# Optimization experiments

Hardware: AMD Instinct MI355X
Metric: run time of the kernel (lower is better)

## Reference

```python
import jax, jax.numpy as jnp
import numpy as np

H = 16
D_MODEL = 1024
D_K = D_MODEL // H


def setup_inputs() -> dict:
    key = jax.random.key(0)
    ks = jax.random.split(key, 12)
    B, S = 2, 2048
    scale = 1.0 / np.sqrt(D_MODEL)
    inp = {
        "query": jax.random.normal(ks[0], (B, S, D_MODEL), jnp.float32),
        "key": jax.random.normal(ks[1], (B, S, D_MODEL), jnp.float32),
        "value": jax.random.normal(ks[2], (B, S, D_MODEL), jnp.float32),
        "mask": jnp.ones((B, 1, S), jnp.int32),
        "Wq": jax.random.normal(ks[3], (D_MODEL, D_MODEL), jnp.float32) * scale,
        "bq": jnp.zeros((D_MODEL,), jnp.float32),
        "Wk": jax.random.normal(ks[4], (D_MODEL, D_MODEL), jnp.float32) * scale,
        "bk": jnp.zeros((D_MODEL,), jnp.float32),
        "Wv": jax.random.normal(ks[5], (D_MODEL, D_MODEL), jnp.float32) * scale,
        "bv": jnp.zeros((D_MODEL,), jnp.float32),
        "Wo": jax.random.normal(ks[6], (D_MODEL, D_MODEL), jnp.float32) * scale,
        "bo": jnp.zeros((D_MODEL,), jnp.float32),
    }
    return inp


def reference(query, key, value, mask, Wq, bq, Wk, bk, Wv, bv, Wo, bo):
    B, S, _ = query.shape
    # QKV projections, split heads: [B, S, D] -> [B, H, S, d_k]
    def proj(x, W, b):
        y = x @ W.T + b
        return y.reshape(B, -1, H, D_K).transpose(0, 2, 1, 3)

    q = proj(query, Wq, bq)
    k = proj(key, Wk, bk)
    v = proj(value, Wv, bv)

    # scaled dot-product attention with full score matrix [B, H, Sq, Sk]
    scores = jnp.einsum("bhqd,bhkd->bhqk", q, k) / np.sqrt(D_K)
    m = mask[:, None, :, :]  # unsqueeze head dim: [B, 1, 1_or_S, S]
    scores = jnp.where(m == 0, jnp.float32(-1e9), scores)
    p_attn = jax.nn.softmax(scores, axis=-1)  # dropout p=0.0 (eval)
    x = jnp.einsum("bhqk,bhkd->bhqd", p_attn, v)

    # merge heads and output projection
    x = x.transpose(0, 2, 1, 3).reshape(B, -1, H * D_K)
    return x @ Wo.T + bo
```

## Files before the change

### kernel.cpp

```cpp
#include <hip/hip_runtime.h>
#include <hip/hip_bf16.h>
#include <stdint.h>

typedef unsigned short us;
typedef __bf16 bf8 __attribute__((ext_vector_type(8)));
typedef float  f4  __attribute__((ext_vector_type(4)));

typedef unsigned int __attribute__((address_space(1))) as1_uint;
typedef unsigned int __attribute__((address_space(3))) as3_uint;

__device__ __forceinline__ void async_ld16(const void* g, void* l) {
    __builtin_amdgcn_global_load_lds((as1_uint*)g, (as3_uint*)l, 16, 0, 0);
}

__device__ __forceinline__ us f2bf(float f) {
    __hip_bfloat16 h = __float2bfloat16(f);
    us u;
    __builtin_memcpy(&u, &h, 2);
    return u;
}

__device__ __forceinline__ unsigned cvt_pk_bf16(float lo, float hi) {
    unsigned r;
    asm("v_cvt_pk_bf16_f32 %0, %1, %2" : "=v"(r) : "v"(lo), "v"(hi));
    return r;
}

__device__ __forceinline__ float fexp2(float x) {
#if __has_builtin(__builtin_amdgcn_exp2f)
    return __builtin_amdgcn_exp2f(x);
#else
    return exp2f(x);
#endif
}

#define SCALE_Q 0.18033688011112042f

__global__ __launch_bounds__(256)
void convert_all(const float* __restrict__ s0, const float* __restrict__ s1,
                 const float* __restrict__ s2, const float* __restrict__ s3,
                 const float* __restrict__ s4, const float* __restrict__ s5,
                 const float* __restrict__ s6,
                 us* __restrict__ d0, us* __restrict__ d1, us* __restrict__ d2,
                 us* __restrict__ d3, us* __restrict__ d4, us* __restrict__ d5,
                 us* __restrict__ d6)
{
    size_t i4 = (((size_t)blockIdx.x * 256) + threadIdx.x) << 2;
    const float* src; us* dst; size_t off;
    if (i4 < ((size_t)3 << 22)) {
        unsigned seg = (unsigned)(i4 >> 22);
        off = i4 & (((size_t)1 << 22) - 1);
        src = seg == 0 ? s0 : (seg == 1 ? s1 : s2);
        dst = seg == 0 ? d0 : (seg == 1 ? d1 : d2);
    } else {
        size_t j = i4 - ((size_t)3 << 22);
        unsigned seg = (unsigned)(j >> 20);
        off = j & (((size_t)1 << 20) - 1);
        src = seg == 0 ? s3 : (seg == 1 ? s4 : (seg == 2 ? s5 : s6));
        dst = seg == 0 ? d3 : (seg == 1 ? d4 : (seg == 2 ? d5 : d6));
    }
    float4 f = *(const float4*)(src + off);
    ushort4 o;
    o.x = f2bf(f.x); o.y = f2bf(f.y); o.z = f2bf(f.z); o.w = f2bf(f.w);
    *(ushort4*)(dst + off) = o;
}

template<int MODE, int BN>
__device__ __forceinline__
void gemm_body(const us* __restrict__ A, const us* __restrict__ W,
               const float* __restrict__ bias, void* __restrict__ out,
               float scale, int bx, int by)
{
    __shared__ us lA[128 * 32];
    __shared__ us lB[BN * 32];

    const int tid  = threadIdx.x;
    const int wv   = tid >> 6;
    const int lane = tid & 63;
    const int l15  = lane & 15;
    const int quad = lane >> 4;
    const int kq   = quad << 3;
    const int cr   = quad << 2;
    const int srow = lane >> 2;
    const int scol = (lane & 3) << 3;
    const int m0   = by << 7;
    const int n0   = bx * BN;
    constexpr int MJ = (BN == 128) ? 4 : 2;
    const int wm = (BN == 128) ? ((wv >> 1) << 6) : (wv << 5);
    const int wn = (BN == 128) ? ((wv & 1) << 6) : 0;

    f4 acc[4][MJ];
    const f4 zero = {0.f, 0.f, 0.f, 0.f};
#pragma unroll
    for (int i = 0; i < 4; ++i)
#pragma unroll
        for (int j = 0; j < MJ; ++j) acc[i][j] = zero;

    for (int kt = 0; kt < 1024; kt += 32) {
#pragma unroll
        for (int s = 0; s < 2; ++s) {
            const int chunk = wv * 2 + s;
            const int row   = chunk * 16 + srow;
            async_ld16(A + (size_t)(m0 + row) * 1024 + kt + scol, &lA[chunk * 512]);
        }
        if (BN == 128) {
#pragma unroll
            for (int s = 0; s < 2; ++s) {
                const int chunk = wv * 2 + s;
                const int row   = chunk * 16 + srow;
                async_ld16(W + (size_t)(n0 + row) * 1024 + kt + scol, &lB[chunk * 512]);
            }
        } else {
            const int row = wv * 16 + srow;
            async_ld16(W + (size_t)(n0 + row) * 1024 + kt + scol, &lB[wv * 512]);
        }
        __syncthreads();

        bf8 wf[4], xf[MJ];
#pragma unroll
        for (int i = 0; i < 4; ++i)
            wf[i] = *(const bf8*)&lB[(wn + i * 16 + l15) * 32 + kq];
#pragma unroll
        for (int j = 0; j < MJ; ++j)
            xf[j] = *(const bf8*)&lA[(wm + j * 16 + l15) * 32 + kq];
#pragma unroll
        for (int i = 0; i < 4; ++i)
#pragma unroll
            for (int j = 0; j < MJ; ++j)
                acc[i][j] = __builtin_amdgcn_mfma_f32_16x16x32_bf16(wf[i], xf[j], acc[i][j], 0, 0, 0);
        __syncthreads();
    }

    if (MODE == 2) {
        us* o = (us*)out;
#pragma unroll
        for (int j = 0; j < MJ; ++j) {
            const int f = m0 + wm + j * 16 + l15;
            const float bf_ = bias[f];
            const int hh = f >> 6, dd = f & 63;
#pragma unroll
            for (int i = 0; i < 4; ++i) {
                const int tokb = n0 + wn + i * 16 + cr;
                const int bb = tokb >> 11, ss_phys = tokb & 2047;
                const int k6 = ss_phys & 63;
                const int kt6 = k6 >> 4, qd = (k6 >> 2) & 3;
                const int c6 = ((kt6 >> 1) << 5) | (qd << 3) | ((kt6 & 1) << 2);
                const int ss = (ss_phys & ~63) | c6;
                us hp[4];
#pragma unroll
                for (int r = 0; r < 4; ++r) hp[r] = f2bf(acc[i][j][r] + bf_);
                uint2 w;
                w.x = (unsigned)hp[0] | ((unsigned)hp[1] << 16);
                w.y = (unsigned)hp[2] | ((unsigned)hp[3] << 16);
                *(uint2*)&o[((size_t)((bb * 16 + hh) * 64 + dd) << 11) + ss] = w;
            }
        }
        return;
    }

#pragma unroll
    for (int i = 0; i < 4; ++i) {
        const int gnb = n0 + wn + i * 16 + cr;
        const f4 bj = *(const f4*)&bias[gnb];
        if (MODE == 0) {
            us* o = (us*)out;
            const int hh = gnb >> 6, dd = gnb & 63;
#pragma unroll
            for (int j = 0; j < MJ; ++j) {
                const int gm = m0 + wm + j * 16 + l15;
                const int bb = gm >> 11, ss = gm & 2047;
                us hp[4];
#pragma unroll
                for (int r = 0; r < 4; ++r)
                    hp[r] = f2bf((acc[i][j][r] + bj[r]) * scale);
                uint2 w;
                w.x = (unsigned)hp[0] | ((unsigned)hp[1] << 16);
                w.y = (unsigned)hp[2] | ((unsigned)hp[3] << 16);
                *(uint2*)&o[(((size_t)(bb * 16 + hh) * 2048 + ss) << 6) + dd] = w;
            }
        } else {
            float* o = (float*)out;
#pragma unroll
            for (int j = 0; j < MJ; ++j) {
                const int gm = m0 + wm + j * 16 + l15;
                f4 v;
#pragma unroll
                for (int r = 0; r < 4; ++r) v[r] = acc[i][j][r] + bj[r];
                *(f4*)&o[((size_t)gm << 10) + gnb] = v;
            }
        }
    }
}

__global__ __launch_bounds__(256)
void gemm_qkv(const us* __restrict__ XQ, const us* __restrict__ XK,
              const us* __restrict__ XV,
              const us* __restrict__ WQ, const us* __restrict__ WK,
              const us* __restrict__ WV,
              const float* __restrict__ bq, const float* __restrict__ bk,
              const float* __restrict__ bv,
              us* __restrict__ QP, us* __restrict__ KP, us* __restrict__ VT)
{
    const int z = blockIdx.z;
    if (z == 2) {
        gemm_body<2, 128>(WV, XV, bv, VT, 1.0f, blockIdx.y, blockIdx.x);
        return;
    }
    const us* A = z == 0 ? XQ : XK;
    const us* W = z == 0 ? WQ : WK;
    const float* b = z == 0 ? bq : bk;
    us* o = z == 0 ? QP : KP;
    const float scale = z == 0 ? SCALE_Q : 1.0f;
    gemm_body<0, 128>(A, W, b, o, scale, blockIdx.x, blockIdx.y);
}

__global__ __launch_bounds__(256)
void gemm_o(const us* __restrict__ A, const us* __restrict__ W,
            const float* __restrict__ bias, float* __restrict__ out)
{
    gemm_body<1, 64>(A, W, bias, out, 1.0f, blockIdx.x, blockIdx.y);
}

__global__ __launch_bounds__(512)
void flash_attn(const us* __restrict__ Qp, const us* __restrict__ Kp,
                const us* __restrict__ Vtp, const int* __restrict__ maskp,
                us* __restrict__ ctx)
{
    __shared__ us lK[2][64 * 64];
    __shared__ us lVt[2][64 * 64];
    __shared__ float lmask[2][64];

    const int tid  = threadIdx.x;
    const int wv   = tid >> 6;
    const int lane = tid & 63;
    const int l15  = lane & 15;
    const int quad = lane >> 4;
    const int cr   = quad << 2;
    const int l7   = l15 & 7;

    const int q0 = blockIdx.x << 8;
    const int h  = blockIdx.y;
    const int b  = blockIdx.z;

    const size_t headoff = ((size_t)(b * 16 + h)) << 17;
    const us* Qh  = Qp  + headoff;
    const us* Kh  = Kp  + headoff;
    const us* Vth = Vtp + headoff;

    const int gr    = lane >> 3;
    const int gslot = ((lane & 7) ^ gr) << 3;

    bf8 qf[2][2];
#pragma unroll
    for (int nt = 0; nt < 2; ++nt)
#pragma unroll
        for (int kb = 0; kb < 2; ++kb)
            qf[nt][kb] = *(const bf8*)(Qh + ((size_t)(q0 + wv * 32 + nt * 16 + l15) << 6)
                                          + kb * 32 + (quad << 3));

    const f4 zero = {0.f, 0.f, 0.f, 0.f};
    f4 of[4][2];
#pragma unroll
    for (int dt = 0; dt < 4; ++dt)
#pragma unroll
        for (int nt = 0; nt < 2; ++nt) of[dt][nt] = zero;
    float li[2] = {0.f, 0.f};

#define FA_ISSUE(kt0, bi)                                                      \
    {                                                                          \
        const int rbase = wv * 8;                                              \
        const int r = rbase + gr;                                              \
        async_ld16(Kh + ((size_t)((kt0) + r) << 6) + gslot,                    \
                   &lK[bi][rbase * 64]);                                       \
        async_ld16(Vth + (size_t)r * 2048 + (kt0) + gslot,                     \
                   &lVt[bi][rbase * 64]);                                      \
        if (tid < 64)                                                          \
            lmask[bi][tid] =                                                   \
                (maskp[((size_t)b << 11) + (kt0) + tid] == 0) ? 0.0f : 1.0f;   \
    }

    FA_ISSUE(0, 0);

    for (int t = 0; t < 32; ++t) {
        const int cur = t & 1;
        __syncthreads();
        if (t < 31) FA_ISSUE((t + 1) * 64, cur ^ 1);

        const us* lKc  = lK[cur];
        const us* lVtc = lVt[cur];

        float rs[2] = {0.f, 0.f};
        unsigned pkx[4][2], pky[4][2];
        __builtin_amdgcn_s_setprio(1);
#pragma unroll
        for (int kt = 0; kt < 4; ++kt) {
            const int krow = (kt * 16 + l15) << 6;
            bf8 kf0 = *(const bf8*)&lKc[krow + ((quad ^ l7) << 3)];
            bf8 kf1 = *(const bf8*)&lKc[krow + (((4 + quad) ^ l7) << 3)];
            f4 st[2];
#pragma unroll
            for (int nt = 0; nt < 2; ++nt) {
                st[nt] = __builtin_amdgcn_mfma_f32_16x16x32_bf16(kf0, qf[nt][0], zero, 0, 0, 0);
                st[nt] = __builtin_amdgcn_mfma_f32_16x16x32_bf16(kf1, qf[nt][1], st[nt], 0, 0, 0);
            }
            const f4 mr = *(const f4*)&lmask[cur][kt * 16 + cr];
#pragma unroll
            for (int nt = 0; nt < 2; ++nt) {
                float p[4];
#pragma unroll
                for (int r = 0; r < 4; ++r) {
                    p[r] = fexp2(st[nt][r]) * mr[r];
                    rs[nt] += p[r];
                }
                pkx[kt][nt] = cvt_pk_bf16(p[0], p[1]);
                pky[kt][nt] = cvt_pk_bf16(p[2], p[3]);
            }
        }
        __builtin_amdgcn_s_setprio(0);
#pragma unroll
        for (int nt = 0; nt < 2; ++nt) {
            float r2 = rs[nt];
            r2 += __shfl_xor(r2, 16, 64);
            r2 += __shfl_xor(r2, 32, 64);
            li[nt] += r2;
        }

        __builtin_amdgcn_s_setprio(1);
#pragma unroll
        for (int kb = 0; kb < 2; ++kb) {
            bf8 pfr[2];
#pragma unroll
            for (int nt = 0; nt < 2; ++nt) {
                uint4 u;
                u.x = pkx[2 * kb][nt];
                u.y = pky[2 * kb][nt];
                u.z = pkx[2 * kb + 1][nt];
                u.w = pky[2 * kb + 1][nt];
                __builtin_memcpy(&pfr[nt], &u, 16);
            }
#pragma unroll
            for (int dt = 0; dt < 4; ++dt) {
                bf8 vf = *(const bf8*)&lVtc[((dt * 16 + l15) << 6) + (((kb * 4 + quad) ^ l7) << 3)];
#pragma unroll
                for (int nt = 0; nt < 2; ++nt)
                    of[dt][nt] = __builtin_amdgcn_mfma_f32_16x16x32_bf16(vf, pfr[nt], of[dt][nt], 0, 0, 0);
            }
        }
        __builtin_amdgcn_s_setprio(0);
    }
#undef FA_ISSUE

#pragma unroll
    for (int nt = 0; nt < 2; ++nt) {
        const float linv = 1.0f / li[nt];
        const int tok = q0 + wv * 32 + nt * 16 + l15;
        const size_t rowb = (((size_t)(b * 2048 + tok)) << 10) + (h << 6);
#pragma unroll
        for (int dt = 0; dt < 4; ++dt) {
            uint2 w;
            w.x = cvt_pk_bf16(of[dt][nt][0] * linv, of[dt][nt][1] * linv);
            w.y = cvt_pk_bf16(of[dt][nt][2] * linv, of[dt][nt][3] * linv);
            *(uint2*)&ctx[rowb + dt * 16 + cr] = w;
        }
    }
}

extern "C" void kernel_launch(void* const* d_in, const int* in_sizes, int n_in,
                              void* d_out, int out_size, void* d_ws, size_t ws_size,
                              hipStream_t stream)
{
    const float* q    = (const float*)d_in[0];
    const float* k    = (const float*)d_in[1];
    const float* v    = (const float*)d_in[2];
    const int*   mask = (const int*)d_in[3];
    const float* Wq   = (const float*)d_in[4];
    const float* bq   = (const float*)d_in[5];
    const float* Wk   = (const float*)d_in[6];
    const float* bk   = (const float*)d_in[7];
    const float* Wv   = (const float*)d_in[8];
    const float* bv   = (const float*)d_in[9];
    const float* Wo   = (const float*)d_in[10];
    const float* bo   = (const float*)d_in[11];
    float* out = (float*)d_out;

    us* ws  = (us*)d_ws;
    us* XQ  = ws;
    us* XK  = ws + 4194304;
    us* XV  = ws + 8388608;
    us* WQb = ws + 12582912;
    us* WKb = ws + 13631488;
    us* WVb = ws + 14680064;
    us* WOb = ws + 15728640;
    us* QP  = ws + 16777216;
    us* KP  = ws + 20971520;
    us* VT  = ws + 25165824;
    us* CTX = XQ;

    convert_all<<<16384, 256, 0, stream>>>(q, k, v, Wq, Wk, Wv, Wo,
                                           XQ, XK, XV, WQb, WKb, WVb, WOb);
    gemm_qkv<<<dim3(8, 32, 3), 256, 0, stream>>>(XQ, XK, XV, WQb, WKb, WVb,
                                                 bq, bk, bv, QP, KP, VT);
    flash_attn<<<dim3(8, 16, 2), 512, 0, stream>>>(QP, KP, VT, mask, CTX);
    gemm_o<<<dim3(16, 32), 256, 0, stream>>>(CTX, WOb, bo, out);
}
```

Measured before the change: 233.3 us.

## Deepen flash-attention K/V pipeline to four LDS stages with vmcnt-based waits

Moves the K/Vt staging in flash_attn from double to quadruple buffering, prefetching two tiles ahead. It replaces __syncthreads with an explicit s_waitcnt vmcnt plus s_barrier, so each wave waits only for the oldest outstanding loads. The whole mask row is converted to float and preloaded into LDS once at kernel start, and the s_setprio hints are dropped. This raises LDS use per block, which may lower occupancy, and the correctness of the vmcnt counts depends on async load ordering.

```diff
diff --git a/kernel.cpp b/kernel.cpp
--- a/kernel.cpp
+++ b/kernel.cpp
@@ -226,9 +226,9 @@
                 const us* __restrict__ Vtp, const int* __restrict__ maskp,
                 us* __restrict__ ctx)
 {
-    __shared__ us lK[2][64 * 64];
-    __shared__ us lVt[2][64 * 64];
-    __shared__ float lmask[2][64];
+    __shared__ us lK[4][64 * 64];
+    __shared__ us lVt[4][64 * 64];
+    __shared__ float lmaskA[2048];
 
     const int tid  = threadIdx.x;
     const int wv   = tid >> 6;
@@ -249,6 +249,16 @@
 
     const int gr    = lane >> 3;
     const int gslot = ((lane & 7) ^ gr) << 3;
+
+    {
+        const int4 mi = *(const int4*)(maskp + ((size_t)b << 11) + (tid << 2));
+        float4 mf;
+        mf.x = mi.x == 0 ? 0.0f : 1.0f;
+        mf.y = mi.y == 0 ? 0.0f : 1.0f;
+        mf.z = mi.z == 0 ? 0.0f : 1.0f;
+        mf.w = mi.w == 0 ? 0.0f : 1.0f;
+        *(float4*)&lmaskA[tid << 2] = mf;
+    }
 
     bf8 qf[2][2];
 #pragma unroll
@@ -274,24 +284,26 @@
                    &lK[bi][rbase * 64]);                                       \
         async_ld16(Vth + (size_t)r * 2048 + (kt0) + gslot,                     \
                    &lVt[bi][rbase * 64]);                                      \
-        if (tid < 64)                                                          \
-            lmask[bi][tid] =                                                   \
-                (maskp[((size_t)b << 11) + (kt0) + tid] == 0) ? 0.0f : 1.0f;   \
-    }
+    }
+
+    __syncthreads();
 
     FA_ISSUE(0, 0);
+    FA_ISSUE(64, 1);
 
     for (int t = 0; t < 32; ++t) {
-        const int cur = t & 1;
-        __syncthreads();
-        if (t < 31) FA_ISSUE((t + 1) * 64, cur ^ 1);
-
-        const us* lKc  = lK[cur];
-        const us* lVtc = lVt[cur];
+        if (t < 31) asm volatile("s_waitcnt vmcnt(2)" ::: "memory");
+        else        asm volatile("s_waitcnt vmcnt(0)" ::: "memory");
+        __builtin_amdgcn_s_barrier();
+        __builtin_amdgcn_sched_barrier(0);
+        if (t < 30) FA_ISSUE((t + 2) * 64, (t + 2) & 3);
+
+        const us* lKc  = lK[t & 3];
+        const us* lVtc = lVt[t & 3];
+        const float* lmt = &lmaskA[t << 6];
 
         float rs[2] = {0.f, 0.f};
         unsigned pkx[4][2], pky[4][2];
-        __builtin_amdgcn_s_setprio(1);
 #pragma unroll
         for (int kt = 0; kt < 4; ++kt) {
             const int krow = (kt * 16 + l15) << 6;
@@ -303,7 +315,7 @@
                 st[nt] = __builtin_amdgcn_mfma_f32_16x16x32_bf16(kf0, qf[nt][0], zero, 0, 0, 0);
                 st[nt] = __builtin_amdgcn_mfma_f32_16x16x32_bf16(kf1, qf[nt][1], st[nt], 0, 0, 0);
             }
-            const f4 mr = *(const f4*)&lmask[cur][kt * 16 + cr];
+            const f4 mr = *(const f4*)&lmt[kt * 16 + cr];
 #pragma unroll
             for (int nt = 0; nt < 2; ++nt) {
                 float p[4];
@@ -316,7 +328,6 @@
                 pky[kt][nt] = cvt_pk_bf16(p[2], p[3]);
             }
         }
-        __builtin_amdgcn_s_setprio(0);
 #pragma unroll
         for (int nt = 0; nt < 2; ++nt) {
             float r2 = rs[nt];
@@ -325,7 +336,6 @@
             li[nt] += r2;
         }
 
-        __builtin_amdgcn_s_setprio(1);
 #pragma unroll
         for (int kb = 0; kb < 2; ++kb) {
             bf8 pfr[2];
@@ -346,7 +356,6 @@
                     of[dt][nt] = __builtin_amdgcn_mfma_f32_16x16x32_bf16(vf, pfr[nt], of[dt][nt], 0, 0, 0);
             }
         }
-        __builtin_amdgcn_s_setprio(0);
     }
 #undef FA_ISSUE
 
```

Result: no change. 234.4 us (+0.5%).
